# Performance work log

Hardware: AMD Instinct MI355X
Metric: run time of the kernel (lower is better)

Reference implementation:

```python
import jax, jax.numpy as jnp
import numpy as np
import math

# normalizer: the module takes it as a callable; we use a standard smooth
# inverse-norm normalizer 1/sqrt(x^2 + eps) applied to the e_inf-like component.
_EPS = 1e-3

def _normalizer(x):
    return 1.0 / jnp.sqrt(x * x + _EPS)


def _dist_vec(tri, basis):
    # tri: (B,H,N,C,5); basis: (5,5,6)
    # vec[...,z] = sum_{x,y} basis[x,y,z] * tri_n[...,x] * tri_n[...,y]
    tri_n = tri * _normalizer(tri[..., 4:5])
    return jnp.einsum('xyz,bhncx,bhncy->bhncz', basis, tri_n, tri_n)


def setup_inputs() -> dict:
    key = jax.random.key(0)
    ks = jax.random.split(key, 8)
    B, H, N, C, S = 1, 8, 4096, 8, 16
    return {
        'q_mv': jax.random.normal(ks[0], (B, H, N, C, 32), jnp.float32),
        'k_mv': jax.random.normal(ks[1], (B, H, N, C, 32), jnp.float32),
        'v_mv': jax.random.normal(ks[2], (B, H, N, C, 32), jnp.float32),
        'q_s': jax.random.normal(ks[3], (B, H, N, S), jnp.float32),
        'k_s': jax.random.normal(ks[4], (B, H, N, S), jnp.float32),
        'v_s': jax.random.normal(ks[5], (B, H, N, S), jnp.float32),
        'basis_q': jax.random.normal(ks[6], (5, 5, 6), jnp.float32),
        'basis_k': jax.random.normal(ks[7], (5, 5, 6), jnp.float32),
    }


def reference(q_mv, k_mv, v_mv, q_s, k_s, v_s, basis_q, basis_k):
    B, H, N, C_qk, _ = q_mv.shape
    C_v = v_mv.shape[-2]
    S_qk = q_s.shape[-1]
    S_v = v_s.shape[-1]
    NUM_IP = 30   # len(_INNER_PRODUCT_WO_EXTREMES_IDX) = indices 1..30
    NUM_DIST = 6
    n_qk = C_qk * (NUM_IP + NUM_DIST) + S_qk
    n_v = C_v * 32 + S_v
    n_ch = 8 * (-(-max(n_qk, n_v) // 8))  # round up to multiple of 8

    # grade-1 components -> distance features
    q_dist = _dist_vec(q_mv[..., 1:6], basis_q)  # (B,H,N,C,6)
    k_dist = _dist_vec(k_mv[..., 1:6], basis_k)

    # inner-product components (indices 1..30)
    q_ip = q_mv[..., 1:31].reshape(B, H, N, C_qk * NUM_IP)
    k_ip = k_mv[..., 1:31].reshape(B, H, N, C_qk * NUM_IP)

    zpad_qk = jnp.zeros((B, H, N, n_ch - n_qk), q_mv.dtype)
    zpad_v = jnp.zeros((B, H, N, n_ch - n_v), v_mv.dtype)

    q = jnp.concatenate([q_ip, q_dist.reshape(B, H, N, -1), q_s, zpad_qk], -1)
    k = jnp.concatenate([k_ip, k_dist.reshape(B, H, N, -1), k_s, zpad_qk], -1)
    v = jnp.concatenate([v_mv.reshape(B, H, N, C_v * 32), v_s, zpad_v], -1)
    k = k * math.sqrt(n_ch / n_qk)

    # standard scaled dot-product attention with scale 1/sqrt(n_ch)
    scale = 1.0 / math.sqrt(n_ch)
    scores = jnp.einsum('bhqd,bhkd->bhqk', q, k) * scale
    attn = jax.nn.softmax(scores, axis=-1)
    v_out = jnp.einsum('bhqk,bhkd->bhqd', attn, v)

    v_out_mv = v_out[..., :C_v * 32].reshape(B, H, N, C_v, 32)
    v_out_s = v_out[..., C_v * 32:C_v * 32 + S_v]
    return (v_out_mv, v_out_s)
```

## Files before the change

### kernel.cpp

```cpp
#include <hip/hip_runtime.h>
#include <math.h>

typedef short bf16x8 __attribute__((ext_vector_type(8)));
typedef float f32x4 __attribute__((ext_vector_type(4)));

#define HH 8
#define NN 4096
#define DIP 256
#define DDX 256
#define DKM 192
#define DV 272
#define BN 32
#define NT (NN/BN)

typedef const __attribute__((address_space(1))) unsigned int* gp_t;
typedef __attribute__((address_space(3))) unsigned int* lp_t;
__device__ __forceinline__ void gload16(const void* g, void* l) {
    __builtin_amdgcn_global_load_lds((gp_t)g, (lp_t)l, 16, 0, 0);
}

__device__ __forceinline__ unsigned short f2bf(float f) {
    unsigned int u = __float_as_uint(f);
    u = (u + 0x7fffu + ((u >> 16) & 1u)) >> 16;
    return (unsigned short)u;
}
__device__ __forceinline__ float bf2f(unsigned short h) {
    return __uint_as_float(((unsigned int)h) << 16);
}

__global__ void feat_kernel(const float* __restrict__ mv,
                            const float* __restrict__ sv,
                            const float* __restrict__ basis,
                            float scale, int qmode,
                            unsigned short* __restrict__ fip,
                            unsigned short* __restrict__ fdx)
{
    __shared__ float sb[150];
    int t = threadIdx.x;
    if (t < 150) sb[t] = basis[t];
    __syncthreads();
    int row = blockIdx.x * 32 + (t >> 3);
    int c = t & 7;
    const float* m = mv + (size_t)row * 256 + c * 32;
    float f[32];
    #pragma unroll
    for (int i = 0; i < 8; ++i) {
        float4 v = ((const float4*)m)[i];
        f[i*4+0] = v.x; f[i*4+1] = v.y; f[i*4+2] = v.z; f[i*4+3] = v.w;
    }
    unsigned short* ip = fip + (size_t)row * DIP;
    unsigned short* dx = fdx + (size_t)row * (qmode ? DDX : DKM);
    #pragma unroll
    for (int j = 0; j < 30; ++j)
        ip[c*30 + j] = f2bf(f[1+j] * scale);
    if (c < 2) {
        #pragma unroll
        for (int i = 0; i < 8; ++i)
            ip[240 + c*8 + i] = f2bf(sv[(size_t)row*16 + c*8 + i] * scale);
    }
    float nn = 1.0f / sqrtf(f[5]*f[5] + 0.001f);
    float tn[5];
    #pragma unroll
    for (int x = 0; x < 5; ++x) tn[x] = f[1+x] * nn;
    #pragma unroll
    for (int z = 0; z < 6; ++z) {
        float acc = 0.f;
        #pragma unroll
        for (int x = 0; x < 5; ++x) {
            #pragma unroll
            for (int y = 0; y < 5; ++y)
                acc = fmaf(sb[(x*5+y)*6 + z] * tn[x], tn[y], acc);
        }
        acc *= scale;
        unsigned short hi = f2bf(acc);
        float r1 = acc - bf2f(hi);
        unsigned short mi = f2bf(r1);
        float r2 = r1 - bf2f(mi);
        unsigned short lo = f2bf(r2);
        int cz = c*6 + z;
        if (qmode) {
            dx[cz]      = hi;  dx[48 + cz]  = hi;
            dx[96 + cz] = mi;  dx[144 + cz] = lo;
            if (cz < 16) { dx[208 + cz] = 0; dx[240 + cz] = 0; }
            if (cz >= 32) { dx[160 + cz] = mi; dx[192 + cz] = hi; }
        } else {
            dx[cz]      = mi;  dx[48 + cz]  = lo;
            dx[96 + cz] = hi;  dx[144 + cz] = hi;
        }
    }
}

__global__ void vtrans_kernel(const float* __restrict__ vmv,
                              const float* __restrict__ vs,
                              unsigned short* __restrict__ dst)
{
    __shared__ unsigned short tile[64][DV];
    int blk = blockIdx.x;
    int h = blk >> 6;
    int n0 = (blk & 63) << 6;
    int t = threadIdx.x;
    #pragma unroll
    for (int it = 0; it < 16; ++it) {
        int v = t + it*256;
        int r = v >> 6;
        int sg = v & 63;
        float4 x = *(const float4*)(vmv + ((size_t)(h*NN + n0 + r))*256 + sg*4);
        tile[r][sg*4+0] = f2bf(x.x);
        tile[r][sg*4+1] = f2bf(x.y);
        tile[r][sg*4+2] = f2bf(x.z);
        tile[r][sg*4+3] = f2bf(x.w);
    }
    #pragma unroll
    for (int it = 0; it < 4; ++it) {
        int v = t + it*256;
        int r = v >> 4;
        int si = v & 15;
        tile[r][256 + si] = f2bf(vs[((size_t)(h*NN + n0 + r))*16 + si]);
    }
    __syncthreads();
    #pragma unroll
    for (int it = 0; it < 17; ++it) {
        int v = t + it*256;
        int dd = v >> 4;
        int sg = v & 15;
        ushort4 o;
        o.x = tile[sg*4+0][dd];
        o.y = tile[sg*4+1][dd];
        o.z = tile[sg*4+2][dd];
        o.w = tile[sg*4+3][dd];
        *(ushort4*)(dst + ((size_t)(h*DV + dd))*NN + n0 + sg*4) = o;
    }
}

__global__ __launch_bounds__(256, 2)
void attn_kernel(const unsigned short* __restrict__ Qip,
                 const unsigned short* __restrict__ Qdx,
                 const unsigned short* __restrict__ Kip,
                 const unsigned short* __restrict__ Kmx,
                 const unsigned short* __restrict__ Vt,
                 float* __restrict__ out)
{
    __shared__ __align__(128) unsigned short smem[39424];

    int blk = blockIdx.x;
    int sbk = ((blk & 7) << 6) | (blk >> 3);
    int h = sbk >> 6;
    int q0 = (sbk & 63) * 64;
    int tid = threadIdx.x;
    int w = tid >> 6;
    int lane = tid & 63;
    int l15 = lane & 15;
    int l4 = lane >> 4;
    int l7l = l15 & 3;
    int l7h = (l15 >> 2) & 1;

    const unsigned short* qipr = Qip + (size_t)(h*NN + q0 + w*16 + l15) * DIP + l4*8;
    const unsigned short* qdxr = Qdx + (size_t)(h*NN + q0 + w*16 + l15) * DDX + l4*8;
    bf16x8 qip[8], qdx[8];
    #pragma unroll
    for (int ks = 0; ks < 8; ++ks) qip[ks] = *(const bf16x8*)(qipr + ks*32);
    #pragma unroll
    for (int ks = 0; ks < 8; ++ks) qdx[ks] = *(const bf16x8*)(qdxr + ks*32);

    int cl16 = (l4 ^ l7l) * 16;
    int kbE = l15*512 + cl16 + l7h*64;
    int kbO = l15*512 + cl16 + 64 - l7h*64;
    int mA  = l15*384 + cl16 + l7h*64;
    int mB  = l15*384 + cl16 + 64 - l7h*64;
    int vbs = 57344 + (l15>>1)*128 + (((((l15&1)<<2) | l4) ^ (l15>>1)) << 4);
    int pbR = 74752 + w*1024 + l15*64;
    int pSeg0 = pbR + ((((l4>>1)    ) ^ l7l) << 4) + (l4&1)*8;
    int pSeg1 = pbR + ((((l4>>1) + 2) ^ l7l) << 4) + (l4&1)*8;
    int pRd   = pbR + ((l4 ^ l7l) << 4);

    int kto0, kto1, kto2, kto3, kmo0, kmo1, kmo2, vto0, vto1, vto2, vto3, vto4;
#define KTFL(SLOT, DST) { int r_ = (SLOT) >> 5, fp_ = (SLOT) & 31; \
    int fl_ = (fp_ & 24) | ((((fp_>>2)&1) ^ ((r_>>2)&1)) << 2) | ((fp_&3) ^ (r_&3)); \
    DST = r_*DIP + fl_*8; }
    KTFL(tid,     kto0) KTFL(tid+256, kto1) KTFL(tid+512, kto2) KTFL(tid+768, kto3)
#define KMFL(SLOT, DST) { int r_ = (SLOT)/24, fp_ = (SLOT)%24; \
    int g_ = fp_>>3, po_ = fp_&7; \
    int pl_ = ((((po_>>2)&1) ^ ((r_>>2)&1)) << 2) | ((po_&3) ^ (r_&3)); \
    DST = r_*DKM + (g_*8 + pl_)*8; }
    KMFL(tid,     kmo0) KMFL(tid+256, kmo1) KMFL(tid+512, kmo2)
#define VTF(SLOT, DST) { int ch_ = (SLOT) >> 3, ws_ = (SLOT) & 7; int lw_ = ws_ ^ (ch_&7); \
    DST = (ch_*2 + (lw_>>2))*NN + (lw_&3)*8; }
    VTF(tid,      vto0) VTF(tid+256,  vto1) VTF(tid+512, vto2)
    VTF(tid+768,  vto3) VTF(tid+1024, vto4)
#undef KTFL
#undef KMFL
#undef VTF

    const unsigned short* kiph = Kip + (size_t)h*NN*DIP;
    const unsigned short* kmxh = Kmx + (size_t)h*NN*DKM;
    const unsigned short* vh   = Vt  + (size_t)h*DV*NN;

    f32x4 zero = {0.f, 0.f, 0.f, 0.f};
    f32x4 oacc[17];
    #pragma unroll
    for (int ct = 0; ct < 17; ++ct) oacc[ct] = zero;
    float mreg = -__builtin_inff();
    float lreg = 0.f;

#define ISSUE_KTMX(TILE, BUF) do { \
    const unsigned short* ks_ = kiph + (size_t)(TILE)*BN*DIP; \
    unsigned short* d0_ = smem + (BUF)*8192 + tid*8; \
    gload16(ks_ + kto0, d0_); \
    gload16(ks_ + kto1, d0_ + 2048); \
    gload16(ks_ + kto2, d0_ + 4096); \
    gload16(ks_ + kto3, d0_ + 6144); \
    const unsigned short* ms_ = kmxh + (size_t)(TILE)*BN*DKM; \
    unsigned short* d1_ = smem + 16384 + (BUF)*6144 + tid*8; \
    gload16(ms_ + kmo0, d1_); \
    gload16(ms_ + kmo1, d1_ + 2048); \
    gload16(ms_ + kmo2, d1_ + 4096); \
} while (0)

#define ISSUE_V(TILE) do { \
    const unsigned short* vs_ = vh + (TILE)*BN; \
    unsigned short* d2_ = smem + 28672 + tid*8; \
    gload16(vs_ + vto0, d2_); \
    gload16(vs_ + vto1, d2_ + 2048); \
    gload16(vs_ + vto2, d2_ + 4096); \
    gload16(vs_ + vto3, d2_ + 6144); \
    if (tid < 64) gload16(vs_ + vto4, d2_ + 8192); \
} while (0)

    ISSUE_KTMX(0, 0);
    int cur = 0;
    #pragma unroll 1
    for (int t = 0; t < NT; ++t) {
        ISSUE_V(t);
        if (w == 0) asm volatile("s_waitcnt vmcnt(5)" ::: "memory");
        else        asm volatile("s_waitcnt vmcnt(4)" ::: "memory");
        __builtin_amdgcn_sched_barrier(0);
        __builtin_amdgcn_s_barrier();
        __builtin_amdgcn_sched_barrier(0);
        if (t < NT-1) ISSUE_KTMX(t+1, cur^1);

        const char* ktb = (const char*)smem + cur*16384;
        const char* kmb = (const char*)smem + 32768 + cur*12288;
        f32x4 sacc[2];
        sacc[0] = zero; sacc[1] = zero;
        __builtin_amdgcn_s_setprio(1);
        #pragma unroll
        for (int ks = 0; ks < 8; ++ks) {
            int off = (ks & 1) ? (kbO + (ks-1)*64) : (kbE + ks*64);
            bf16x8 a0 = *(const bf16x8*)(ktb + off);
            bf16x8 a1 = *(const bf16x8*)(ktb + off + 8192);
            sacc[0] = __builtin_amdgcn_mfma_f32_16x16x32_bf16(a0, qip[ks], sacc[0], 0, 0, 0);
            sacc[1] = __builtin_amdgcn_mfma_f32_16x16x32_bf16(a1, qip[ks], sacc[1], 0, 0, 0);
        }
        #pragma unroll
        for (int ct = 0; ct < 2; ++ct) {
            const char* kk = kmb + ct*6144;
            bf16x8 ka0 = *(const bf16x8*)(kk + mA);
            bf16x8 ka1 = *(const bf16x8*)(kk + mB);
            bf16x8 ka2 = *(const bf16x8*)(kk + mA + 128);
            bf16x8 kb0 = *(const bf16x8*)(kk + mB + 128);
            bf16x8 kb1 = *(const bf16x8*)(kk + mA + 256);
            bf16x8 kb2 = *(const bf16x8*)(kk + mB + 256);
            f32x4 a = sacc[ct];
            a = __builtin_amdgcn_mfma_f32_16x16x32_bf16(ka0, qdx[0], a, 0, 0, 0);
            a = __builtin_amdgcn_mfma_f32_16x16x32_bf16(ka1, qdx[1], a, 0, 0, 0);
            a = __builtin_amdgcn_mfma_f32_16x16x32_bf16(ka2, qdx[2], a, 0, 0, 0);
            a = __builtin_amdgcn_mfma_f32_16x16x32_bf16(kb0, qdx[3], a, 0, 0, 0);
            a = __builtin_amdgcn_mfma_f32_16x16x32_bf16(kb1, qdx[4], a, 0, 0, 0);
            a = __builtin_amdgcn_mfma_f32_16x16x32_bf16(kb2, qdx[5], a, 0, 0, 0);
            a = __builtin_amdgcn_mfma_f32_16x16x32_bf16(ka0, qdx[3], a, 0, 0, 0);
            a = __builtin_amdgcn_mfma_f32_16x16x32_bf16(ka1, qdx[6], a, 0, 0, 0);
            a = __builtin_amdgcn_mfma_f32_16x16x32_bf16(kb0, qdx[0], a, 0, 0, 0);
            a = __builtin_amdgcn_mfma_f32_16x16x32_bf16(kb1, qdx[7], a, 0, 0, 0);
            sacc[ct] = a;
        }
        __builtin_amdgcn_s_setprio(0);

        float pm = fmaxf(fmaxf(fmaxf(sacc[0][0], sacc[0][1]), fmaxf(sacc[0][2], sacc[0][3])),
                         fmaxf(fmaxf(sacc[1][0], sacc[1][1]), fmaxf(sacc[1][2], sacc[1][3])));
        pm = fmaxf(pm, __shfl_xor(pm, 16, 64));
        pm = fmaxf(pm, __shfl_xor(pm, 32, 64));
        if (!__all(pm <= mreg + 8.0f)) {
            float mnew = fmaxf(mreg, pm);
            float al = __expf(mreg - mnew);
            mreg = mnew;
            lreg *= al;
            float a0 = __shfl(al, l4*4+0, 64);
            float a1 = __shfl(al, l4*4+1, 64);
            float a2 = __shfl(al, l4*4+2, 64);
            float a3 = __shfl(al, l4*4+3, 64);
            #pragma unroll
            for (int ct = 0; ct < 17; ++ct) {
                oacc[ct][0] *= a0; oacc[ct][1] *= a1;
                oacc[ct][2] *= a2; oacc[ct][3] *= a3;
            }
        }
        float p0 = __expf(sacc[0][0] - mreg), p1 = __expf(sacc[0][1] - mreg);
        float p2 = __expf(sacc[0][2] - mreg), p3 = __expf(sacc[0][3] - mreg);
        float p4 = __expf(sacc[1][0] - mreg), p5 = __expf(sacc[1][1] - mreg);
        float p6 = __expf(sacc[1][2] - mreg), p7 = __expf(sacc[1][3] - mreg);
        lreg += ((p0 + p1) + (p2 + p3)) + ((p4 + p5) + (p6 + p7));
        unsigned r01, r23, r45, r67;
        asm("v_cvt_pk_bf16_f32 %0, %1, %2" : "=v"(r01) : "v"(p0), "v"(p1));
        asm("v_cvt_pk_bf16_f32 %0, %1, %2" : "=v"(r23) : "v"(p2), "v"(p3));
        asm("v_cvt_pk_bf16_f32 %0, %1, %2" : "=v"(r45) : "v"(p4), "v"(p5));
        asm("v_cvt_pk_bf16_f32 %0, %1, %2" : "=v"(r67) : "v"(p6), "v"(p7));
        {
            char* pbp = (char*)smem;
            *(unsigned*)(pbp + pSeg0 + 0) = r01;
            *(unsigned*)(pbp + pSeg0 + 4) = r23;
            *(unsigned*)(pbp + pSeg1 + 0) = r45;
            *(unsigned*)(pbp + pSeg1 + 4) = r67;
        }

        if (t < NT-1) asm volatile("s_waitcnt vmcnt(7)" ::: "memory");
        else          asm volatile("s_waitcnt vmcnt(0)" ::: "memory");
        __builtin_amdgcn_sched_barrier(0);
        __builtin_amdgcn_s_barrier();
        __builtin_amdgcn_sched_barrier(0);

        {
            bf16x8 pa = *(const bf16x8*)((const char*)smem + pRd);
            __builtin_amdgcn_s_setprio(1);
            #pragma unroll
            for (int ct = 0; ct < 17; ++ct) {
                bf16x8 bv = *(const bf16x8*)((const char*)smem + vbs + ct*1024);
                oacc[ct] = __builtin_amdgcn_mfma_f32_16x16x32_bf16(pa, bv, oacc[ct], 0, 0, 0);
            }
            __builtin_amdgcn_s_setprio(0);
        }
        __builtin_amdgcn_s_barrier();
        __builtin_amdgcn_sched_barrier(0);
        cur ^= 1;
    }
#undef ISSUE_KTMX
#undef ISSUE_V

    float lf = lreg;
    lf += __shfl_xor(lf, 16, 64);
    lf += __shfl_xor(lf, 32, 64);
    const size_t mv_total = (size_t)HH * NN * 256;
    #pragma unroll
    for (int j = 0; j < 4; ++j) {
        float inv = 1.0f / __shfl(lf, l4*4 + j, 64);
        int q = q0 + w*16 + l4*4 + j;
        float* po = out + ((size_t)h*NN + q) * 256 + l15;
        #pragma unroll
        for (int ct = 0; ct < 16; ++ct)
            po[ct*16] = oacc[ct][j] * inv;
        out[mv_total + ((size_t)h*NN + q)*16 + l15] = oacc[16][j] * inv;
    }
}

extern "C" void kernel_launch(void* const* d_in, const int* in_sizes, int n_in,
                              void* d_out, int out_size, void* d_ws, size_t ws_size,
                              hipStream_t stream)
{
    const float* q_mv = (const float*)d_in[0];
    const float* k_mv = (const float*)d_in[1];
    const float* v_mv = (const float*)d_in[2];
    const float* q_s  = (const float*)d_in[3];
    const float* k_s  = (const float*)d_in[4];
    const float* v_s  = (const float*)d_in[5];
    const float* basis_q = (const float*)d_in[6];
    const float* basis_k = (const float*)d_in[7];
    float* out = (float*)d_out;

    unsigned short* qip = (unsigned short*)d_ws;
    unsigned short* qdx = qip + (size_t)HH*NN*DIP;
    unsigned short* kip = qdx + (size_t)HH*NN*DDX;
    unsigned short* kmx = kip + (size_t)HH*NN*DIP;
    unsigned short* vt  = kmx + (size_t)HH*NN*DKM;

    const float qscale = 0.05735393346764042f;

    feat_kernel<<<dim3(1024), dim3(256), 0, stream>>>(q_mv, q_s, basis_q, qscale, 1, qip, qdx);
    feat_kernel<<<dim3(1024), dim3(256), 0, stream>>>(k_mv, k_s, basis_k, 1.0f,   0, kip, kmx);
    vtrans_kernel<<<dim3(512), dim3(256), 0, stream>>>(v_mv, v_s, vt);
    attn_kernel<<<dim3(512), dim3(256), 0, stream>>>(qip, qdx, kip, kmx, vt, out);
}
```

Measured before the change: 315.0 us.

## Use 512-thread blocks of 128 queries and double-buffer V tiles

The attention kernel now runs 8 waves per block covering 128 queries, so each K/V tile loaded into shared memory is shared by twice as many query rows. V is now double-buffered and prefetched together with the next K tiles, which removes the mid-iteration wait and barrier that used to sit before the PV MFMAs. Shared memory per block grows, only one block fits per CU, and the grid halves to 256 blocks, which may leave some CUs idle.

```diff
diff --git a/kernel.cpp b/kernel.cpp
--- a/kernel.cpp
+++ b/kernel.cpp
@@ -132,7 +132,7 @@
     }
 }
 
-__global__ __launch_bounds__(256, 2)
+__global__ __launch_bounds__(512, 1)
 void attn_kernel(const unsigned short* __restrict__ Qip,
                  const unsigned short* __restrict__ Qdx,
                  const unsigned short* __restrict__ Kip,
@@ -140,12 +140,12 @@
                  const unsigned short* __restrict__ Vt,
                  float* __restrict__ out)
 {
-    __shared__ __align__(128) unsigned short smem[39424];
+    __shared__ __align__(128) unsigned short smem[50176];
 
     int blk = blockIdx.x;
-    int sbk = ((blk & 7) << 6) | (blk >> 3);
-    int h = sbk >> 6;
-    int q0 = (sbk & 63) * 64;
+    int sbk = ((blk & 7) << 5) | (blk >> 3);
+    int h = sbk >> 5;
+    int q0 = (sbk & 31) * 128;
     int tid = threadIdx.x;
     int w = tid >> 6;
     int lane = tid & 63;
@@ -167,26 +167,27 @@
     int kbO = l15*512 + cl16 + 64 - l7h*64;
     int mA  = l15*384 + cl16 + l7h*64;
     int mB  = l15*384 + cl16 + 64 - l7h*64;
-    int vbs = 57344 + (l15>>1)*128 + (((((l15&1)<<2) | l4) ^ (l15>>1)) << 4);
-    int pbR = 74752 + w*1024 + l15*64;
+    int vlane = (l15>>1)*128 + (((((l15&1)<<2) | l4) ^ (l15>>1)) << 4);
+    int pbR = 92160 + w*1024 + l15*64;
     int pSeg0 = pbR + ((((l4>>1)    ) ^ l7l) << 4) + (l4&1)*8;
     int pSeg1 = pbR + ((((l4>>1) + 2) ^ l7l) << 4) + (l4&1)*8;
     int pRd   = pbR + ((l4 ^ l7l) << 4);
 
-    int kto0, kto1, kto2, kto3, kmo0, kmo1, kmo2, vto0, vto1, vto2, vto3, vto4;
+    int kt0s, kt1s, km0s, km1vt, vt1s, vt2s;
 #define KTFL(SLOT, DST) { int r_ = (SLOT) >> 5, fp_ = (SLOT) & 31; \
     int fl_ = (fp_ & 24) | ((((fp_>>2)&1) ^ ((r_>>2)&1)) << 2) | ((fp_&3) ^ (r_&3)); \
     DST = r_*DIP + fl_*8; }
-    KTFL(tid,     kto0) KTFL(tid+256, kto1) KTFL(tid+512, kto2) KTFL(tid+768, kto3)
 #define KMFL(SLOT, DST) { int r_ = (SLOT)/24, fp_ = (SLOT)%24; \
     int g_ = fp_>>3, po_ = fp_&7; \
     int pl_ = ((((po_>>2)&1) ^ ((r_>>2)&1)) << 2) | ((po_&3) ^ (r_&3)); \
     DST = r_*DKM + (g_*8 + pl_)*8; }
-    KMFL(tid,     kmo0) KMFL(tid+256, kmo1) KMFL(tid+512, kmo2)
 #define VTF(SLOT, DST) { int ch_ = (SLOT) >> 3, ws_ = (SLOT) & 7; int lw_ = ws_ ^ (ch_&7); \
     DST = (ch_*2 + (lw_>>2))*NN + (lw_&3)*8; }
-    VTF(tid,      vto0) VTF(tid+256,  vto1) VTF(tid+512, vto2)
-    VTF(tid+768,  vto3) VTF(tid+1024, vto4)
+    KTFL(tid, kt0s) KTFL(tid+512, kt1s)
+    KMFL(tid, km0s)
+    if (tid < 256) { KMFL(tid+512, km1vt) } else { VTF(tid-256, km1vt) }
+    VTF(tid+256, vt1s)
+    VTF(tid+768, vt2s)
 #undef KTFL
 #undef KMFL
 #undef VTF
@@ -202,44 +203,40 @@
     float mreg = -__builtin_inff();
     float lreg = 0.f;
 
-#define ISSUE_KTMX(TILE, BUF) do { \
+#define ISSUE(TILE, BUF) do { \
     const unsigned short* ks_ = kiph + (size_t)(TILE)*BN*DIP; \
-    unsigned short* d0_ = smem + (BUF)*8192 + tid*8; \
-    gload16(ks_ + kto0, d0_); \
-    gload16(ks_ + kto1, d0_ + 2048); \
-    gload16(ks_ + kto2, d0_ + 4096); \
-    gload16(ks_ + kto3, d0_ + 6144); \
     const unsigned short* ms_ = kmxh + (size_t)(TILE)*BN*DKM; \
-    unsigned short* d1_ = smem + 16384 + (BUF)*6144 + tid*8; \
-    gload16(ms_ + kmo0, d1_); \
-    gload16(ms_ + kmo1, d1_ + 2048); \
-    gload16(ms_ + kmo2, d1_ + 4096); \
+    const unsigned short* vs_ = vh + (TILE)*BN; \
+    unsigned short* ktd_ = smem + (BUF)*8192; \
+    unsigned short* kmd_ = smem + 16384 + (BUF)*6144; \
+    unsigned short* vtd_ = smem + 28672 + (BUF)*8704; \
+    gload16(ks_ + kt0s, ktd_ + tid*8); \
+    gload16(ks_ + kt1s, ktd_ + (tid+512)*8); \
+    gload16(ms_ + km0s, kmd_ + tid*8); \
+    if (tid < 256) gload16(ms_ + km1vt, kmd_ + (512+tid)*8); \
+    else           gload16(vs_ + km1vt, vtd_ + (tid-256)*8); \
+    gload16(vs_ + vt1s, vtd_ + (tid+256)*8); \
+    if (tid < 320) gload16(vs_ + vt2s, vtd_ + (tid+768)*8); \
 } while (0)
 
-#define ISSUE_V(TILE) do { \
-    const unsigned short* vs_ = vh + (TILE)*BN; \
-    unsigned short* d2_ = smem + 28672 + tid*8; \
-    gload16(vs_ + vto0, d2_); \
-    gload16(vs_ + vto1, d2_ + 2048); \
-    gload16(vs_ + vto2, d2_ + 4096); \
-    gload16(vs_ + vto3, d2_ + 6144); \
-    if (tid < 64) gload16(vs_ + vto4, d2_ + 8192); \
-} while (0)
-
-    ISSUE_KTMX(0, 0);
+    ISSUE(0, 0);
     int cur = 0;
     #pragma unroll 1
     for (int t = 0; t < NT; ++t) {
-        ISSUE_V(t);
-        if (w == 0) asm volatile("s_waitcnt vmcnt(5)" ::: "memory");
-        else        asm volatile("s_waitcnt vmcnt(4)" ::: "memory");
+        if (t < NT-1) ISSUE(t+1, cur^1);
+        if (t < NT-1) {
+            if (w < 5) asm volatile("s_waitcnt vmcnt(6)" ::: "memory");
+            else       asm volatile("s_waitcnt vmcnt(5)" ::: "memory");
+        } else {
+            asm volatile("s_waitcnt vmcnt(0)" ::: "memory");
+        }
         __builtin_amdgcn_sched_barrier(0);
         __builtin_amdgcn_s_barrier();
         __builtin_amdgcn_sched_barrier(0);
-        if (t < NT-1) ISSUE_KTMX(t+1, cur^1);
 
         const char* ktb = (const char*)smem + cur*16384;
         const char* kmb = (const char*)smem + 32768 + cur*12288;
+        const char* vtb = (const char*)smem + 57344 + cur*17408;
         f32x4 sacc[2];
         sacc[0] = zero; sacc[1] = zero;
         __builtin_amdgcn_s_setprio(1);
@@ -312,18 +309,12 @@
             *(unsigned*)(pbp + pSeg1 + 4) = r67;
         }
 
-        if (t < NT-1) asm volatile("s_waitcnt vmcnt(7)" ::: "memory");
-        else          asm volatile("s_waitcnt vmcnt(0)" ::: "memory");
-        __builtin_amdgcn_sched_barrier(0);
-        __builtin_amdgcn_s_barrier();
-        __builtin_amdgcn_sched_barrier(0);
-
         {
             bf16x8 pa = *(const bf16x8*)((const char*)smem + pRd);
             __builtin_amdgcn_s_setprio(1);
             #pragma unroll
             for (int ct = 0; ct < 17; ++ct) {
-                bf16x8 bv = *(const bf16x8*)((const char*)smem + vbs + ct*1024);
+                bf16x8 bv = *(const bf16x8*)(vtb + vlane + ct*1024);
                 oacc[ct] = __builtin_amdgcn_mfma_f32_16x16x32_bf16(pa, bv, oacc[ct], 0, 0, 0);
             }
             __builtin_amdgcn_s_setprio(0);
@@ -332,8 +323,7 @@
         __builtin_amdgcn_sched_barrier(0);
         cur ^= 1;
     }
-#undef ISSUE_KTMX
-#undef ISSUE_V
+#undef ISSUE
 
     float lf = lreg;
     lf += __shfl_xor(lf, 16, 64);
@@ -376,5 +366,5 @@
     feat_kernel<<<dim3(1024), dim3(256), 0, stream>>>(q_mv, q_s, basis_q, qscale, 1, qip, qdx);
     feat_kernel<<<dim3(1024), dim3(256), 0, stream>>>(k_mv, k_s, basis_k, 1.0f,   0, kip, kmx);
     vtrans_kernel<<<dim3(512), dim3(256), 0, stream>>>(v_mv, v_s, vt);
-    attn_kernel<<<dim3(512), dim3(256), 0, stream>>>(qip, qdx, kip, kmx, vt, out);
-}
+    attn_kernel<<<dim3(256), dim3(512), 0, stream>>>(qip, qdx, kip, kmx, vt, out);
+}
```

Result: slower. 325.4 us (+3.3%).
